# Performance work log

Measured on AMD Instinct MI355X. Metric: run time of the kernel, lower is better.

## Reference

```python
import jax, jax.numpy as jnp
import numpy as np


def setup_inputs() -> dict:
    key = jax.random.key(0)
    ks = jax.random.split(key, 8)
    B, C, H, W = 4, 256, 64, 64
    Ci = C // 8  # inter_channels = 32
    x = jax.random.normal(ks[0], (B, C, H, W), dtype=jnp.float32)
    # 1x1 conv weights stored as [out, in] matrices (kernel size 1)
    sq = 1.0 / np.sqrt(C)
    Wq = jax.random.uniform(ks[1], (Ci, C), jnp.float32, -sq, sq)
    bq = jax.random.uniform(ks[2], (Ci,), jnp.float32, -sq, sq)
    Wk = jax.random.uniform(ks[3], (Ci, C), jnp.float32, -sq, sq)
    bk = jax.random.uniform(ks[4], (Ci,), jnp.float32, -sq, sq)
    Wv = jax.random.uniform(ks[5], (C, C), jnp.float32, -sq, sq)
    bv = jax.random.uniform(ks[6], (C,), jnp.float32, -sq, sq)
    # torch initializes gamma to zeros; use a nonzero value so output depends on attention path
    gamma = jnp.array([0.5], dtype=jnp.float32)
    return {"x": x, "Wq": Wq, "bq": bq, "Wk": Wk, "bk": bk, "Wv": Wv, "bv": bv, "gamma": gamma}


def reference(x, Wq, bq, Wk, bk, Wv, bv, gamma):
    B, C, H, W = x.shape
    N = H * W
    xf = x.reshape(B, C, N)                        # [B, C, N]
    # 1x1 convs == channel-mixing matmuls
    q = jnp.einsum('oc,bcn->bon', Wq, xf) + bq[None, :, None]   # [B, Ci, N]
    k = jnp.einsum('oc,bcn->bon', Wk, xf) + bk[None, :, None]   # [B, Ci, N]
    v = jnp.einsum('oc,bcn->bon', Wv, xf) + bv[None, :, None]   # [B, C,  N]
    # energy[b, n, m] = sum_c q[b, c, n] * k[b, c, m]  (no scaling, per DANet)
    energy = jnp.einsum('bcn,bcm->bnm', q, k)      # [B, N, N]
    attention = jax.nn.softmax(energy, axis=-1)    # softmax over keys m
    # out[b, c, n] = sum_m v[b, c, m] * attention[b, n, m]
    out = jnp.einsum('bcm,bnm->bcn', v, attention)
    out = out.reshape(B, C, H, W)
    return gamma[0] * out + x
```

## Files before the change

kernel.cpp:

```cpp
#include <hip/hip_runtime.h>
#include <hip/hip_bf16.h>
#include <math.h>

typedef __bf16 bf16x8 __attribute__((ext_vector_type(8)));
typedef float  floatx4 __attribute__((ext_vector_type(4)));
typedef float  floatx16 __attribute__((ext_vector_type(16)));
typedef unsigned u32x2 __attribute__((ext_vector_type(2)));

#define MFMA(a, b, c)   __builtin_amdgcn_mfma_f32_16x16x32_bf16((a), (b), (c), 0, 0, 0)
#define MFMA32(a, b, c) __builtin_amdgcn_mfma_f32_32x32x16_bf16((a), (b), (c), 0, 0, 0)

__device__ __forceinline__ unsigned short f2bf(float f) {
  union { float f; unsigned u; } v; v.f = f;
  unsigned r = v.u + 0x7FFFu + ((v.u >> 16) & 1u);
  return (unsigned short)(r >> 16);
}
__device__ __forceinline__ float bf2f(unsigned short u) {
  union { unsigned u; float f; } v; v.u = ((unsigned)u) << 16;
  return v.f;
}
__device__ __forceinline__ unsigned pack2(float a, float b) {
  __bf16 x = (__bf16)a, y = (__bf16)b;
  unsigned short ux = __builtin_bit_cast(unsigned short, x);
  unsigned short uy = __builtin_bit_cast(unsigned short, y);
  return (unsigned)ux | ((unsigned)uy << 16);
}
__device__ __forceinline__ float exp2_fast(float x) {
#if __has_builtin(__builtin_amdgcn_exp2f)
  return __builtin_amdgcn_exp2f(x);
#else
  return exp2f(x);
#endif
}

__global__ __launch_bounds__(256) void k_wconv(const float* __restrict__ Wq,
                                               const float* __restrict__ Wk,
                                               const float* __restrict__ Wv,
                                               unsigned short* __restrict__ Wall) {
  int i = blockIdx.x * 256 + threadIdx.x;
  int o = i >> 8, c = i & 255;
  float v = (o < 32) ? Wq[o * 256 + c]
          : (o < 64) ? Wk[(o - 32) * 256 + c]
                     : Wv[(o - 64) * 256 + c];
  Wall[i] = f2bf(v);
}

__global__ __launch_bounds__(256) void k_projx(const float* __restrict__ x,
                                               const unsigned short* __restrict__ Wall,
                                               const float* __restrict__ bq,
                                               const float* __restrict__ bk,
                                               const float* __restrict__ bv,
                                               unsigned short* __restrict__ qbf,
                                               unsigned short* __restrict__ kbf,
                                               unsigned short* __restrict__ vbf) {
  int b = blockIdx.x >> 8;
  int m0 = (blockIdx.x & 255) * 16;
  int tid = threadIdx.x;
  int qr = tid >> 6;
  int lane = tid & 63;
  int l15 = lane & 15, quad = lane >> 4;

  __shared__ alignas(16) unsigned short xs[16][264];
  __shared__ alignas(16) unsigned short Os[4][64][24];

  {
    const float* xrow = x + ((size_t)b * 256 + tid) * 4096 + m0;
#pragma unroll
    for (int g = 0; g < 4; ++g) {
      float4 d = *(const float4*)(xrow + g * 4);
      xs[g * 4 + 0][tid] = f2bf(d.x);
      xs[g * 4 + 1][tid] = f2bf(d.y);
      xs[g * 4 + 2][tid] = f2bf(d.z);
      xs[g * 4 + 3][tid] = f2bf(d.w);
    }
  }
  __syncthreads();

  floatx4 acc[5];
#pragma unroll
  for (int tt = 0; tt < 5; ++tt) acc[tt] = floatx4{0.f, 0.f, 0.f, 0.f};

#pragma unroll
  for (int ks = 0; ks < 8; ++ks) {
    bf16x8 a = *(const bf16x8*)&xs[l15][ks * 32 + quad * 8];
    {
      bf16x8 w = *(const bf16x8*)(Wall + (size_t)(qr * 16 + l15) * 256 + ks * 32 + quad * 8);
      acc[0] = MFMA(a, w, acc[0]);
    }
#pragma unroll
    for (int t = 0; t < 4; ++t) {
      int gt = 4 + qr * 4 + t;
      bf16x8 w = *(const bf16x8*)(Wall + (size_t)(gt * 16 + l15) * 256 + ks * 32 + quad * 8);
      acc[1 + t] = MFMA(a, w, acc[1 + t]);
    }
  }
  {
    int o = qr * 16 + l15;
    float bias = (o < 32) ? bq[o] : bk[o - 32];
    float scale = (o < 32) ? 1.44269504088896340736f : 1.0f;
    unsigned short* dst = (o < 32) ? qbf : kbf;
    int oc = o & 31;
    int kh = oc >> 4, h2 = (oc >> 3) & 1, c8 = oc & 7;
#pragma unroll
    for (int r = 0; r < 4; ++r) {
      int m = m0 + quad * 4 + r;
      dst[(size_t)b * 131072 + (size_t)(m >> 5) * 1024 + kh * 512 + h2 * 256 +
          (m & 31) * 8 + c8] = f2bf((acc[0][r] + bias) * scale);
    }
  }
#pragma unroll
  for (int t = 0; t < 4; ++t) {
    int lr = t * 16 + l15;
    int c = qr * 64 + lr;
    float bias = bv[c];
#pragma unroll
    for (int r = 0; r < 4; ++r)
      Os[qr][lr][quad * 4 + r] = f2bf(acc[1 + t][r] + bias);
  }
  __syncthreads();
  {
    int kb = m0 >> 5, kk = (m0 >> 4) & 1;
#pragma unroll
    for (int i = 0; i < 2; ++i) {
      int idx = lane + 64 * i;
      int r = idx >> 1, g = idx & 1;
      int c = qr * 64 + r;
      int cb = c >> 5, ch = c & 31;
      *(uint4*)(vbf + (size_t)b * 1048576 + (size_t)kb * 8192 +
                (size_t)cb * 1024 + kk * 512 + g * 256 + ch * 8) =
          *(const uint4*)&Os[qr][r][g * 8];
    }
  }
}

__device__ __forceinline__ void softmax_pack(floatx16 st, float& lp, bf16x8 (&pa)[2], int hi) {
  float p[16];
#pragma unroll
  for (int r = 0; r < 16; ++r) p[r] = exp2_fast(st[r]);
  lp += (((p[0] + p[1]) + (p[2] + p[3])) + ((p[4] + p[5]) + (p[6] + p[7]))) +
        (((p[8] + p[9]) + (p[10] + p[11])) + ((p[12] + p[13]) + (p[14] + p[15])));
  unsigned d0[4], d1[4];
#pragma unroll
  for (int t = 0; t < 4; ++t) {
    d0[t] = pack2(p[4 * t + 0], p[4 * t + 1]);
    d1[t] = pack2(p[4 * t + 2], p[4 * t + 3]);
  }
#pragma unroll
  for (int ks = 0; ks < 2; ++ks) {
#if __has_builtin(__builtin_amdgcn_permlane32_swap)
    (void)hi;
    u32x2 r0 = __builtin_amdgcn_permlane32_swap(d0[2 * ks], d0[2 * ks + 1], false, false);
    u32x2 r1 = __builtin_amdgcn_permlane32_swap(d1[2 * ks], d1[2 * ks + 1], false, false);
    union { unsigned u[4]; bf16x8 v; } u;
    u.u[0] = r0[0]; u.u[1] = r1[0]; u.u[2] = r0[1]; u.u[3] = r1[1];
    pa[ks] = u.v;
#else
    unsigned s0 = hi ? d0[2 * ks] : d0[2 * ks + 1];
    unsigned s1 = hi ? d1[2 * ks] : d1[2 * ks + 1];
    unsigned o0 = (unsigned)__shfl_xor((int)s0, 32);
    unsigned o1 = (unsigned)__shfl_xor((int)s1, 32);
    union { unsigned u[4]; bf16x8 v; } u;
    u.u[0] = hi ? o0 : d0[2 * ks];
    u.u[1] = hi ? o1 : d1[2 * ks];
    u.u[2] = hi ? d0[2 * ks + 1] : o0;
    u.u[3] = hi ? d1[2 * ks + 1] : o1;
    pa[ks] = u.v;
#endif
  }
}

__global__ __launch_bounds__(256, 4) void k_attn(const unsigned short* __restrict__ qbf,
                                                 const unsigned short* __restrict__ kbf,
                                                 const unsigned short* __restrict__ vbf,
                                                 const float* __restrict__ x,
                                                 const float* __restrict__ gma,
                                                 float* __restrict__ out) {
  int wg = (blockIdx.x & 7) * 256 + (blockIdx.x >> 3);
  const int qb = wg & 127;
  const int g  = wg >> 7;
  const int cz = g & 3;
  const int b  = g >> 2;
  const int s  = threadIdx.x >> 6;
  const int lane = threadIdx.x & 63;
  const int l31 = lane & 31;
  const int hi  = lane >> 5;
  const int q0  = qb * 32;

  __shared__ float lpL[4][32];
  __shared__ float ltot[32];
  __shared__ alignas(16) unsigned short Ol[4][64][40];

  const floatx16 z16 = {0.f, 0.f, 0.f, 0.f, 0.f, 0.f, 0.f, 0.f,
                        0.f, 0.f, 0.f, 0.f, 0.f, 0.f, 0.f, 0.f};

  bf16x8 qf[2];
  {
    const unsigned short* qbase =
        qbf + (size_t)b * 131072 + (size_t)qb * 1024 + hi * 256 + l31 * 8;
    qf[0] = *(const bf16x8*)(qbase);
    qf[1] = *(const bf16x8*)(qbase + 512);
  }

  floatx16 acc[2];
  acc[0] = z16; acc[1] = z16;

  float lp = 0.f;

  const unsigned short* krow =
      kbf + (size_t)b * 131072 + (size_t)(s * 32) * 1024 + hi * 256 + l31 * 8;
  const unsigned short* vrow =
      vbf + (size_t)b * 1048576 + (size_t)(s * 32) * 8192 + (size_t)(cz * 2) * 1024 +
      hi * 256 + l31 * 8;

  bf16x8 kf0 = *(const bf16x8*)krow;
  bf16x8 kf1 = *(const bf16x8*)(krow + 512);

  for (int it = 0; it < 32; ++it) {
    bf16x8 vb[2][2];
    const unsigned short* vit = vrow + (size_t)it * 8192;
#pragma unroll
    for (int ct = 0; ct < 2; ++ct) {
      vb[ct][0] = *(const bf16x8*)(vit + ct * 1024);
      vb[ct][1] = *(const bf16x8*)(vit + ct * 1024 + 512);
    }

    floatx16 st = MFMA32(kf0, qf[0], z16);
    st = MFMA32(kf1, qf[1], st);

    const unsigned short* kn = krow + (size_t)((it + 1) & 31) * 1024;
    kf0 = *(const bf16x8*)kn;
    kf1 = *(const bf16x8*)(kn + 512);

    bf16x8 pa[2];
    softmax_pack(st, lp, pa, hi);

    __builtin_amdgcn_s_setprio(1);
#pragma unroll
    for (int ct = 0; ct < 2; ++ct) {
      acc[ct] = MFMA32(pa[0], vb[ct][0], acc[ct]);
      acc[ct] = MFMA32(pa[1], vb[ct][1], acc[ct]);
    }
    __builtin_amdgcn_s_setprio(0);
  }

  lp += __shfl_xor(lp, 32);
  if (hi == 0) lpL[s][l31] = lp;

#pragma unroll
  for (int ct = 0; ct < 2; ++ct) {
#pragma unroll
    for (int gi = 0; gi < 4; ++gi) {
      unsigned w0 = pack2(acc[ct][4 * gi + 0], acc[ct][4 * gi + 1]);
      unsigned w1 = pack2(acc[ct][4 * gi + 2], acc[ct][4 * gi + 3]);
      unsigned long long w = (unsigned long long)w0 | ((unsigned long long)w1 << 32);
      *(unsigned long long*)&Ol[s][ct * 32 + l31][8 * gi + 4 * hi] = w;
    }
  }
  __syncthreads();
  if (threadIdx.x < 32) {
    int q = threadIdx.x;
    ltot[q] = (lpL[0][q] + lpL[1][q]) + (lpL[2][q] + lpL[3][q]);
  }
  __syncthreads();

  {
    const float gv = gma[0];
    int ch = threadIdx.x >> 2;
    int qg = threadIdx.x & 3;
    float o[8];
#pragma unroll
    for (int j = 0; j < 8; ++j) o[j] = 0.f;
#pragma unroll
    for (int sp = 0; sp < 4; ++sp) {
      uint4 a0 = *(const uint4*)&Ol[sp][ch][qg * 8];
      unsigned uu[4] = {a0.x, a0.y, a0.z, a0.w};
#pragma unroll
      for (int jj = 0; jj < 4; ++jj) {
        o[2 * jj + 0] += bf2f((unsigned short)(uu[jj] & 0xffffu));
        o[2 * jj + 1] += bf2f((unsigned short)(uu[jj] >> 16));
      }
    }
    size_t rowa = ((size_t)b * 256 + cz * 64 + ch) * 4096 + q0 + qg * 8;
    const float* xrow = x + rowa;
    float* orow = out + rowa;
#pragma unroll
    for (int j4 = 0; j4 < 2; ++j4) {
      float4 xv = *(const float4*)(xrow + j4 * 4);
      float4 r;
      r.x = xv.x + gv * o[j4 * 4 + 0] / ltot[qg * 8 + j4 * 4 + 0];
      r.y = xv.y + gv * o[j4 * 4 + 1] / ltot[qg * 8 + j4 * 4 + 1];
      r.z = xv.z + gv * o[j4 * 4 + 2] / ltot[qg * 8 + j4 * 4 + 2];
      r.w = xv.w + gv * o[j4 * 4 + 3] / ltot[qg * 8 + j4 * 4 + 3];
      *(float4*)(orow + j4 * 4) = r;
    }
  }
}

extern "C" void kernel_launch(void* const* d_in, const int* in_sizes, int n_in,
                              void* d_out, int out_size, void* d_ws, size_t ws_size,
                              hipStream_t stream) {
  const float* x   = (const float*)d_in[0];
  const float* Wq  = (const float*)d_in[1];
  const float* bq  = (const float*)d_in[2];
  const float* Wk  = (const float*)d_in[3];
  const float* bk  = (const float*)d_in[4];
  const float* Wv  = (const float*)d_in[5];
  const float* bv  = (const float*)d_in[6];
  const float* gma = (const float*)d_in[7];
  float* out = (float*)d_out;

  unsigned short* qbf  = (unsigned short*)d_ws;
  unsigned short* kbf  = qbf + (size_t)4 * 131072;
  unsigned short* vbf  = kbf + (size_t)4 * 131072;
  unsigned short* Wall = vbf + (size_t)4 * 1048576;

  k_wconv<<<320, 256, 0, stream>>>(Wq, Wk, Wv, Wall);
  k_projx<<<1024, 256, 0, stream>>>(x, Wall, bq, bk, bv, qbf, kbf, vbf);
  k_attn<<<2048, 256, 0, stream>>>(qbf, kbf, vbf, x, gma, out);
}
```

Before: 177.5 us.

## Widen attention channel tile to 128 and coalesce projection input loads

The attention kernel now has each workgroup accumulate 128 output channels instead of 64, with four accumulators per wave. This halves how many times the QK^T scores and exponentials are recomputed per query block, and halves the grid size. The cost is more registers per wave, so the occupancy hint drops from 4 to 3, and there is a larger LDS reduction buffer. The projection kernel now loads x so that groups of threads read contiguous 16-float row segments, and it drops a block barrier before the per-wave LDS readback, relying on wave-local ordering.

```diff
diff --git a/kernel.cpp b/kernel.cpp
--- a/kernel.cpp
+++ b/kernel.cpp
@@ -54,7 +54,8 @@
                                                unsigned short* __restrict__ kbf,
                                                unsigned short* __restrict__ vbf) {
   int b = blockIdx.x >> 8;
-  int m0 = (blockIdx.x & 255) * 16;
+  int nt = blockIdx.x & 255;
+  int m0 = nt * 16;
   int tid = threadIdx.x;
   int qr = tid >> 6;
   int lane = tid & 63;
@@ -64,14 +65,17 @@
   __shared__ alignas(16) unsigned short Os[4][64][24];
 
   {
-    const float* xrow = x + ((size_t)b * 256 + tid) * 4096 + m0;
-#pragma unroll
-    for (int g = 0; g < 4; ++g) {
-      float4 d = *(const float4*)(xrow + g * 4);
-      xs[g * 4 + 0][tid] = f2bf(d.x);
-      xs[g * 4 + 1][tid] = f2bf(d.y);
-      xs[g * 4 + 2][tid] = f2bf(d.z);
-      xs[g * 4 + 3][tid] = f2bf(d.w);
+    int g = tid & 3;
+    int r0 = tid >> 2;
+    const float* xcol = x + (size_t)b * 256 * 4096 + m0 + g * 4;
+#pragma unroll
+    for (int pass = 0; pass < 4; ++pass) {
+      int r = pass * 64 + r0;
+      float4 d = *(const float4*)(xcol + (size_t)r * 4096);
+      xs[g * 4 + 0][r] = f2bf(d.x);
+      xs[g * 4 + 1][r] = f2bf(d.y);
+      xs[g * 4 + 2][r] = f2bf(d.z);
+      xs[g * 4 + 3][r] = f2bf(d.w);
     }
   }
   __syncthreads();
@@ -117,9 +121,8 @@
     for (int r = 0; r < 4; ++r)
       Os[qr][lr][quad * 4 + r] = f2bf(acc[1 + t][r] + bias);
   }
-  __syncthreads();
-  {
-    int kb = m0 >> 5, kk = (m0 >> 4) & 1;
+  {
+    int kb = nt >> 1, kk = nt & 1;
 #pragma unroll
     for (int i = 0; i < 2; ++i) {
       int idx = lane + 64 * i;
@@ -169,26 +172,27 @@
   }
 }
 
-__global__ __launch_bounds__(256, 4) void k_attn(const unsigned short* __restrict__ qbf,
+__global__ __launch_bounds__(256, 3) void k_attn(const unsigned short* __restrict__ qbf,
                                                  const unsigned short* __restrict__ kbf,
                                                  const unsigned short* __restrict__ vbf,
                                                  const float* __restrict__ x,
                                                  const float* __restrict__ gma,
                                                  float* __restrict__ out) {
-  int wg = (blockIdx.x & 7) * 256 + (blockIdx.x >> 3);
+  int wg = (blockIdx.x & 7) * 128 + (blockIdx.x >> 3);
   const int qb = wg & 127;
   const int g  = wg >> 7;
-  const int cz = g & 3;
-  const int b  = g >> 2;
-  const int s  = threadIdx.x >> 6;
-  const int lane = threadIdx.x & 63;
+  const int cw = g & 1;
+  const int b  = g >> 1;
+  const int tid = threadIdx.x;
+  const int s  = tid >> 6;
+  const int lane = tid & 63;
   const int l31 = lane & 31;
   const int hi  = lane >> 5;
   const int q0  = qb * 32;
 
   __shared__ float lpL[4][32];
   __shared__ float ltot[32];
-  __shared__ alignas(16) unsigned short Ol[4][64][40];
+  __shared__ alignas(16) unsigned short Ol[4][128][40];
 
   const floatx16 z16 = {0.f, 0.f, 0.f, 0.f, 0.f, 0.f, 0.f, 0.f,
                         0.f, 0.f, 0.f, 0.f, 0.f, 0.f, 0.f, 0.f};
@@ -201,25 +205,26 @@
     qf[1] = *(const bf16x8*)(qbase + 512);
   }
 
-  floatx16 acc[2];
-  acc[0] = z16; acc[1] = z16;
+  floatx16 acc[4];
+#pragma unroll
+  for (int j = 0; j < 4; ++j) acc[j] = z16;
 
   float lp = 0.f;
 
   const unsigned short* krow =
       kbf + (size_t)b * 131072 + (size_t)(s * 32) * 1024 + hi * 256 + l31 * 8;
   const unsigned short* vrow =
-      vbf + (size_t)b * 1048576 + (size_t)(s * 32) * 8192 + (size_t)(cz * 2) * 1024 +
+      vbf + (size_t)b * 1048576 + (size_t)(s * 32) * 8192 + (size_t)(cw * 4) * 1024 +
       hi * 256 + l31 * 8;
 
   bf16x8 kf0 = *(const bf16x8*)krow;
   bf16x8 kf1 = *(const bf16x8*)(krow + 512);
 
   for (int it = 0; it < 32; ++it) {
-    bf16x8 vb[2][2];
+    bf16x8 vb[4][2];
     const unsigned short* vit = vrow + (size_t)it * 8192;
 #pragma unroll
-    for (int ct = 0; ct < 2; ++ct) {
+    for (int ct = 0; ct < 4; ++ct) {
       vb[ct][0] = *(const bf16x8*)(vit + ct * 1024);
       vb[ct][1] = *(const bf16x8*)(vit + ct * 1024 + 512);
     }
@@ -236,7 +241,7 @@
 
     __builtin_amdgcn_s_setprio(1);
 #pragma unroll
-    for (int ct = 0; ct < 2; ++ct) {
+    for (int ct = 0; ct < 4; ++ct) {
       acc[ct] = MFMA32(pa[0], vb[ct][0], acc[ct]);
       acc[ct] = MFMA32(pa[1], vb[ct][1], acc[ct]);
     }
@@ -247,7 +252,7 @@
   if (hi == 0) lpL[s][l31] = lp;
 
 #pragma unroll
-  for (int ct = 0; ct < 2; ++ct) {
+  for (int ct = 0; ct < 4; ++ct) {
 #pragma unroll
     for (int gi = 0; gi < 4; ++gi) {
       unsigned w0 = pack2(acc[ct][4 * gi + 0], acc[ct][4 * gi + 1]);
@@ -257,40 +262,42 @@
     }
   }
   __syncthreads();
-  if (threadIdx.x < 32) {
-    int q = threadIdx.x;
+  if (tid < 32) {
+    int q = tid;
     ltot[q] = (lpL[0][q] + lpL[1][q]) + (lpL[2][q] + lpL[3][q]);
   }
   __syncthreads();
 
   {
     const float gv = gma[0];
-    int ch = threadIdx.x >> 2;
-    int qg = threadIdx.x & 3;
-    float o[8];
-#pragma unroll
-    for (int j = 0; j < 8; ++j) o[j] = 0.f;
+    int ch = tid >> 1;
+    int qh = tid & 1;
+    int qoff = qh * 16;
+    float o[16];
+#pragma unroll
+    for (int j = 0; j < 16; ++j) o[j] = 0.f;
 #pragma unroll
     for (int sp = 0; sp < 4; ++sp) {
-      uint4 a0 = *(const uint4*)&Ol[sp][ch][qg * 8];
-      unsigned uu[4] = {a0.x, a0.y, a0.z, a0.w};
-#pragma unroll
-      for (int jj = 0; jj < 4; ++jj) {
+      const uint4* p = (const uint4*)&Ol[sp][ch][qh * 16];
+      uint4 a0 = p[0], a1 = p[1];
+      unsigned uu[8] = {a0.x, a0.y, a0.z, a0.w, a1.x, a1.y, a1.z, a1.w};
+#pragma unroll
+      for (int jj = 0; jj < 8; ++jj) {
         o[2 * jj + 0] += bf2f((unsigned short)(uu[jj] & 0xffffu));
         o[2 * jj + 1] += bf2f((unsigned short)(uu[jj] >> 16));
       }
     }
-    size_t rowa = ((size_t)b * 256 + cz * 64 + ch) * 4096 + q0 + qg * 8;
+    size_t rowa = ((size_t)b * 256 + cw * 128 + ch) * 4096 + q0 + qoff;
     const float* xrow = x + rowa;
     float* orow = out + rowa;
 #pragma unroll
-    for (int j4 = 0; j4 < 2; ++j4) {
+    for (int j4 = 0; j4 < 4; ++j4) {
       float4 xv = *(const float4*)(xrow + j4 * 4);
       float4 r;
-      r.x = xv.x + gv * o[j4 * 4 + 0] / ltot[qg * 8 + j4 * 4 + 0];
-      r.y = xv.y + gv * o[j4 * 4 + 1] / ltot[qg * 8 + j4 * 4 + 1];
-      r.z = xv.z + gv * o[j4 * 4 + 2] / ltot[qg * 8 + j4 * 4 + 2];
-      r.w = xv.w + gv * o[j4 * 4 + 3] / ltot[qg * 8 + j4 * 4 + 3];
+      r.x = xv.x + gv * o[j4 * 4 + 0] / ltot[qoff + j4 * 4 + 0];
+      r.y = xv.y + gv * o[j4 * 4 + 1] / ltot[qoff + j4 * 4 + 1];
+      r.z = xv.z + gv * o[j4 * 4 + 2] / ltot[qoff + j4 * 4 + 2];
+      r.w = xv.w + gv * o[j4 * 4 + 3] / ltot[qoff + j4 * 4 + 3];
       *(float4*)(orow + j4 * 4) = r;
     }
   }
@@ -316,5 +323,5 @@
 
   k_wconv<<<320, 256, 0, stream>>>(Wq, Wk, Wv, Wall);
   k_projx<<<1024, 256, 0, stream>>>(x, Wall, bq, bk, bv, qbf, kbf, vbf);
-  k_attn<<<2048, 256, 0, stream>>>(qbf, kbf, vbf, x, gma, out);
-}
+  k_attn<<<1024, 256, 0, stream>>>(qbf, kbf, vbf, x, gma, out);
+}
```

Result: faster. 164.6 us (-7.2%).
